# Kernel optimization log

Measured on AMD Instinct MI355X. Metric: run time of the kernel, lower is better.

The kernel has to match this reference:

```python
import jax, jax.numpy as jnp
import numpy as np

D_MODEL = 1024
HEAD = 16
D_K = D_MODEL // HEAD


def setup_inputs() -> dict:
    key = jax.random.key(0)
    ks = jax.random.split(key, 6)
    B, S = 2, 2048
    scale = 1.0 / np.sqrt(D_MODEL)
    return {
        "q": jax.random.normal(ks[0], (B, S, D_MODEL), dtype=jnp.float32),
        "k": jax.random.normal(ks[1], (B, S, D_MODEL), dtype=jnp.float32),
        "v": jax.random.normal(ks[2], (B, S, D_MODEL), dtype=jnp.float32),
        "W_q": jax.random.normal(ks[3], (D_MODEL, D_MODEL), dtype=jnp.float32) * scale,
        "W_k": jax.random.normal(ks[4], (D_MODEL, D_MODEL), dtype=jnp.float32) * scale,
        "W_v": jax.random.normal(ks[5], (D_MODEL, D_MODEL), dtype=jnp.float32) * scale,
    }


def reference(q, k, v, W_q, W_k, W_v):
    B, S, _ = q.shape
    # nn.Linear: y = x @ W.T ; then split heads (B,S,H,dk) -> (B,H,S,dk) -> (B*H,S,dk)
    def proj(x, W):
        y = jnp.einsum('bsd,ed->bse', x, W)
        return y.reshape(B, S, HEAD, D_K).transpose(0, 2, 1, 3).reshape(B * HEAD, S, D_K)

    qh = proj(q, W_q)
    kh = proj(k, W_k)
    vh = proj(v, W_v)

    scores = jnp.einsum('nsd,ntd->nst', qh, kh) / np.sqrt(D_K).astype(np.float32)
    attn = jax.nn.softmax(scores, axis=2)
    out = jnp.einsum('nst,ntd->nsd', attn, vh)  # (B*H, S, dk), flat index = b*H + h

    # Faithful torch.chunk(dim=0, head) + torch.cat(dim=2):
    # chunk c = rows [c*B:(c+1)*B]; concatenated along feature dim.
    out = out.reshape(HEAD, B, S, D_K).transpose(1, 2, 0, 3).reshape(B, S, D_MODEL)
    return out
```

## Files before the change

### kernel.cpp

```cpp
#include <hip/hip_runtime.h>
#include <hip/hip_bf16.h>
#include <stdint.h>

typedef unsigned short u16;
typedef __attribute__((ext_vector_type(8))) short bf16x8;
typedef __attribute__((ext_vector_type(8))) _Float16 f16x8;
typedef __attribute__((ext_vector_type(4))) float f32x4;
typedef __attribute__((ext_vector_type(4))) u16 u16x4;
typedef __attribute__((ext_vector_type(4))) float f4v;

#define DEV __device__ __forceinline__

DEV u16 f2bf(float x) {
    union { float f; uint32_t u; } v; v.f = x;
    uint32_t r = v.u + 0x7FFF + ((v.u >> 16) & 1);
    return (u16)(r >> 16);
}

DEV float fexp2(float x) {
    float r;
    asm("v_exp_f32 %0, %1" : "=v"(r) : "v"(x));
    return r;
}

DEV f32x4 mfma16(bf16x8 a, bf16x8 b, f32x4 c) {
    return __builtin_amdgcn_mfma_f32_16x16x32_bf16(a, b, c, 0, 0, 0);
}
DEV f32x4 mfma16h(f16x8 a, f16x8 b, f32x4 c) {
    return __builtin_amdgcn_mfma_f32_16x16x32_f16(a, b, c, 0, 0, 0);
}

DEV void gld_lds16(const u16* g, u16* lds) {
    __builtin_amdgcn_global_load_lds(
        (const __attribute__((address_space(1))) void*)g,
        (__attribute__((address_space(3))) void*)lds, 16, 0, 0);
}

#define VMCNT2 asm volatile("s_waitcnt vmcnt(2)" ::: "memory")
#define VMCNT0 asm volatile("s_waitcnt vmcnt(0)" ::: "memory")
#define BAR() __builtin_amdgcn_s_barrier()

DEV u16 h2u(_Float16 h) { union { _Float16 h; u16 u; } v; v.h = h; return v.u; }

struct PrepArgs {
    const float* src[6];
    u16* dst[6];
    int n4[6];
};

__global__ __launch_bounds__(256) void prep_kernel(PrepArgs a) {
    const int z = blockIdx.y;
    const f4v* __restrict__ src = (const f4v*)a.src[z];
    u16x4* __restrict__ dst = (u16x4*)a.dst[z];
    const int n4 = a.n4[z];
    int i = blockIdx.x * blockDim.x + threadIdx.x;
    const int stride = gridDim.x * blockDim.x;
    for (; i < n4; i += stride) {
        f4v x = src[i];
        u16x4 d;
#pragma unroll
        for (int c = 0; c < 4; ++c) d[c] = h2u((_Float16)x[c]);
        dst[i] = d;
    }
}

struct ProjArgs {
    const u16* xf[3];
    const u16* wf[3];
    u16* outq;
    u16* outk;
    u16* outvt;
};

__global__ __launch_bounds__(512, 2) void proj_kernel(ProjArgs args) {
    __shared__ u16 lds[2][32768];

    const int tid = threadIdx.x;
    const int w = tid >> 6, l = tid & 63;
    const int fr = l & 15, fg = l >> 4;
    const int wa = w >> 2, wb = w & 3;

    const int b0 = blockIdx.x;
    const int swz = (b0 & 7) * 24 + (b0 >> 3);
    const int z = swz >> 6;
    const int r = swz & 63;

    int ta, tb;
    const u16 *A0, *B0;
    if (z < 2) {
        ta = r & 3; tb = r >> 2;
        A0 = args.wf[z];
        B0 = args.xf[z];
    } else {
        ta = r >> 2; tb = r & 3;
        A0 = args.xf[2];
        B0 = args.wf[2];
    }

    const int s_r = tid >> 3;
    const int s_c = (((tid & 7) ^ (s_r & 7)) << 3);
    const size_t aoff = (size_t)(ta * 256 + s_r) * 1024 + s_c;
    const size_t boff = (size_t)(tb * 256 + s_r) * 1024 + s_c;

    const int abase = (wa * 128 + fr) * 64;
    const int bbase = 16384 + (wb * 64 + fr) * 64;
    const int sl0 = ((fg) ^ (fr & 7)) << 3;
    const int sl1 = ((4 + fg) ^ (fr & 7)) << 3;

    f32x4 acc[8][4];
#pragma unroll
    for (int mi = 0; mi < 8; ++mi)
#pragma unroll
        for (int ni = 0; ni < 4; ++ni)
            acc[mi][ni] = (f32x4){0.f, 0.f, 0.f, 0.f};

#define STAGE2(SRC, OFFBASE, REGION, HALF, BUFN, KTN)                               \
    do {                                                                            \
        _Pragma("unroll")                                                           \
        for (int j = 0; j < 2; ++j) {                                               \
            gld_lds16((SRC) + (OFFBASE) + (size_t)((HALF) * 128 + j * 64) * 1024    \
                           + (size_t)(KTN) * 64,                                    \
                      &lds[BUFN][(REGION) + (HALF) * 8192 + j * 4096 + w * 512]);   \
        }                                                                           \
    } while (0)

#pragma unroll
    for (int h = 0; h < 2; ++h) {
#pragma unroll
        for (int j = 0; j < 2; ++j) {
            gld_lds16(A0 + aoff + (size_t)(h * 128 + j * 64) * 1024,
                      &lds[0][h * 8192 + j * 4096 + w * 512]);
            gld_lds16(B0 + boff + (size_t)(h * 128 + j * 64) * 1024,
                      &lds[0][16384 + h * 8192 + j * 4096 + w * 512]);
        }
    }

#define PHASE(MQ0, STAGECALL)                                                       \
    do {                                                                            \
        if (more) STAGECALL;                                                        \
        f16x8 p00 = *(const f16x8*)&Lb[abase + (MQ0) * 1024 + sl0];                 \
        f16x8 p01 = *(const f16x8*)&Lb[abase + (MQ0) * 1024 + sl1];                 \
        f16x8 p10 = *(const f16x8*)&Lb[abase + (MQ0 + 1) * 1024 + sl0];             \
        f16x8 p11 = *(const f16x8*)&Lb[abase + (MQ0 + 1) * 1024 + sl1];             \
        BAR();                                                                      \
        __builtin_amdgcn_s_setprio(1);                                              \
        _Pragma("unroll")                                                           \
        for (int ni = 0; ni < 4; ++ni) {                                            \
            acc[MQ0][ni] = mfma16h(p00, Bf0[ni], acc[MQ0][ni]);                     \
            acc[MQ0][ni] = mfma16h(p01, Bf1[ni], acc[MQ0][ni]);                     \
            acc[MQ0 + 1][ni] = mfma16h(p10, Bf0[ni], acc[MQ0 + 1][ni]);             \
            acc[MQ0 + 1][ni] = mfma16h(p11, Bf1[ni], acc[MQ0 + 1][ni]);             \
        }                                                                           \
        __builtin_amdgcn_s_setprio(0);                                              \
        BAR();                                                                      \
    } while (0)

#pragma unroll 1
    for (int t = 0; t < 16; ++t) {
        const int buf = t & 1;
        const int nbuf = buf ^ 1;
        const int tn = t + 1;
        const bool more = (tn < 16);
        const int ktn = tn;
        const u16* An = A0;
        const u16* Bn = B0;
        const u16* Lb = &lds[buf][0];

        f16x8 Bf0[4], Bf1[4];

        if (more) STAGE2(An, aoff, 0, 0, nbuf, ktn);
        if (more) { VMCNT2; } else { VMCNT0; }
        BAR();
        {
            f16x8 a00 = *(const f16x8*)&Lb[abase + sl0];
            f16x8 a01 = *(const f16x8*)&Lb[abase + sl1];
            f16x8 a10 = *(const f16x8*)&Lb[abase + 1024 + sl0];
            f16x8 a11 = *(const f16x8*)&Lb[abase + 1024 + sl1];
#pragma unroll
            for (int ni = 0; ni < 4; ++ni) {
                Bf0[ni] = *(const f16x8*)&Lb[bbase + ni * 1024 + sl0];
                Bf1[ni] = *(const f16x8*)&Lb[bbase + ni * 1024 + sl1];
            }
            BAR();
            __builtin_amdgcn_s_setprio(1);
#pragma unroll
            for (int ni = 0; ni < 4; ++ni) {
                acc[0][ni] = mfma16h(a00, Bf0[ni], acc[0][ni]);
                acc[0][ni] = mfma16h(a01, Bf1[ni], acc[0][ni]);
                acc[1][ni] = mfma16h(a10, Bf0[ni], acc[1][ni]);
                acc[1][ni] = mfma16h(a11, Bf1[ni], acc[1][ni]);
            }
            __builtin_amdgcn_s_setprio(0);
            BAR();
        }
        PHASE(2, STAGE2(An, aoff, 0, 1, nbuf, ktn));
        PHASE(4, STAGE2(Bn, boff, 16384, 0, nbuf, ktn));
        PHASE(6, STAGE2(Bn, boff, 16384, 1, nbuf, ktn));
    }
#undef PHASE
#undef STAGE2

    if (z < 2) {
        u16* outp = (z == 0) ? args.outq : args.outk;
        const float osc = (z == 0) ? 0.18033688011112f : 1.0f;
#pragma unroll
        for (int mq = 0; mq < 8; ++mq) {
#pragma unroll
            for (int ni = 0; ni < 4; ++ni) {
                const int e0 = ta * 256 + wa * 128 + mq * 16 + fg * 4;
                const int m = tb * 256 + wb * 64 + ni * 16 + fr;
                const int n = (m >> 11) * 16 + (e0 >> 6);
                const int s = m & 2047;
                u16x4 pk;
#pragma unroll
                for (int rr = 0; rr < 4; ++rr) pk[rr] = f2bf(acc[mq][ni][rr] * osc);
                *(u16x4*)&outp[((size_t)(n * 2048 + s)) * 64 + (e0 & 63)] = pk;
            }
        }
    } else {
        u16* outp = args.outvt;
#pragma unroll
        for (int mq = 0; mq < 8; ++mq) {
#pragma unroll
            for (int ni = 0; ni < 4; ++ni) {
                const int m0 = ta * 256 + wa * 128 + mq * 16 + fg * 4;
                const int e = tb * 256 + wb * 64 + ni * 16 + fr;
                const int n = (m0 >> 11) * 16 + (e >> 6);
                u16x4 pk;
#pragma unroll
                for (int rr = 0; rr < 4; ++rr) pk[rr] = f2bf(acc[mq][ni][rr]);
                *(u16x4*)&outp[((size_t)(n * 64 + (e & 63))) * 2048 + (m0 & 2047)] = pk;
            }
        }
    }
}

__global__ __launch_bounds__(512, 8) void attn_kernel(const u16* __restrict__ qh,
                                                      const u16* __restrict__ kh,
                                                      const u16* __restrict__ vt,
                                                      float* __restrict__ out) {
    __shared__ u16 lds[2][8192];

    const int tid = threadIdx.x;
    const int w = tid >> 6, l = tid & 63;
    const int fr = l & 15, fg = l >> 4;

    const int b = blockIdx.x;
    const int n = (b & 7) * 4 + ((b >> 3) >> 4);
    const int qt = (b >> 3) & 15;
    const int qbase = qt * 128 + w * 16;

    const u16* khn = kh + (size_t)n * 2048 * 64;
    const u16* vtn = vt + (size_t)n * 64 * 2048;

    const u16* qrow = qh + ((size_t)n * 2048 + qbase + fr) * 64;
    bf16x8 aq0 = *(const bf16x8*)(qrow + fg * 8);
    bf16x8 aq1 = *(const bf16x8*)(qrow + 32 + fg * 8);

    const int srow = tid >> 3;
    const int sch = tid & 7;
    const int kg_s = (srow & 3) + 4 * ((srow >> 3) & 1);
    const int kws = ((sch + kg_s) & 7) * 8;
    const int vg_s = srow & 7;
    const int vws = ((sch + vg_s) & 7) * 8;

    const int rbase = ((fr >> 2) << 3) + (fr & 3);
    const int kg_r = (fr & 3) + 4 * ((fr >> 2) & 1);
    const int ksl0 = ((fg + kg_r) & 7) * 8;
    const int ksl1 = ((fg + 4 + kg_r) & 7) * 8;
    const int vg_r = fr & 7;
    const int vsl0 = ((fg + vg_r) & 7) * 8;
    const int vsl1 = ((4 + fg + vg_r) & 7) * 8;

    f32x4 acc[4];
#pragma unroll
    for (int dc = 0; dc < 4; ++dc) acc[dc] = (f32x4){0.f, 0.f, 0.f, 0.f};
    float lsum = 0.f;

    bf16x8 kr0, vr0;

#define STAGE_LOAD(c_) do {                                                        \
        kr0 = *(const bf16x8*)(khn + (size_t)((c_) * 64 + srow) * 64 + sch * 8);   \
        vr0 = *(const bf16x8*)(vtn + (size_t)srow * 2048 + (c_) * 64 + sch * 8);   \
    } while (0)

#define STAGE_WRITE(buf_) do {                                                     \
        *(bf16x8*)&lds[buf_][srow * 64 + kws] = kr0;                               \
        *(bf16x8*)&lds[buf_][4096 + srow * 64 + vws] = vr0;                        \
    } while (0)

    STAGE_LOAD(0);
    STAGE_WRITE(0);
    STAGE_LOAD(1);
    __syncthreads();

    for (int c = 0; c < 32; ++c) {
        const int cur = c & 1;
        const u16* Kb = &lds[cur][0];
        const u16* Vb = &lds[cur][4096];

        f32x4 sf[4];
        __builtin_amdgcn_s_setprio(1);
#pragma unroll
        for (int cc = 0; cc < 4; ++cc) {
            const int rr = ((cc >> 1) << 5) + ((cc & 1) << 2) + rbase;
            f32x4 s = (f32x4){0.f, 0.f, 0.f, 0.f};
            s = mfma16(*(const bf16x8*)&Kb[rr * 64 + ksl0], aq0, s);
            s = mfma16(*(const bf16x8*)&Kb[rr * 64 + ksl1], aq1, s);
            sf[cc] = s;
        }
        __builtin_amdgcn_s_setprio(0);

        f32x4 ps = (f32x4){0.f, 0.f, 0.f, 0.f};
#pragma unroll
        for (int cc = 0; cc < 4; ++cc) {
#pragma unroll
            for (int rr = 0; rr < 4; ++rr)
                sf[cc][rr] = fexp2(sf[cc][rr]);
            ps += sf[cc];
        }
        lsum += (ps[0] + ps[1]) + (ps[2] + ps[3]);

        if (c < 31) {
            STAGE_WRITE(cur ^ 1);
            if (c < 30) STAGE_LOAD(c + 2);
        }

        __builtin_amdgcn_s_setprio(1);
#pragma unroll
        for (int pw = 0; pw < 2; ++pw) {
            union { bf16x8 v; uint32_t u[4]; } ap;
#pragma unroll
            for (int q2 = 0; q2 < 4; ++q2) {
                float lo = sf[2 * pw + (q2 >> 1)][(q2 & 1) * 2 + 0];
                float hi = sf[2 * pw + (q2 >> 1)][(q2 & 1) * 2 + 1];
                asm("v_cvt_pk_bf16_f32 %0, %1, %2" : "=v"(ap.u[q2]) : "v"(lo), "v"(hi));
            }
            const int vsl = pw ? vsl1 : vsl0;
#pragma unroll
            for (int dc = 0; dc < 4; ++dc)
                acc[dc] = mfma16(*(const bf16x8*)&Vb[(dc * 16 + fr) * 64 + vsl],
                                 ap.v, acc[dc]);
        }
        __builtin_amdgcn_s_setprio(0);

        if (c < 31) __syncthreads();
    }

    lsum += __shfl_xor(lsum, 16, 64);
    lsum += __shfl_xor(lsum, 32, 64);

    const float inv = 1.f / lsum;
    const int bq = n & 1;
    const int col0 = (n >> 1) * 64;
    float* orow = out + ((size_t)bq * 2048 + qbase + fr) * 1024 + col0 + fg * 4;
#pragma unroll
    for (int dblk = 0; dblk < 4; ++dblk) {
        f4v o;
#pragma unroll
        for (int rr = 0; rr < 4; ++rr) o[rr] = acc[dblk][rr] * inv;
        *(f4v*)&orow[dblk * 16] = o;
    }
#undef STAGE_LOAD
#undef STAGE_WRITE
}

extern "C" void kernel_launch(void* const* d_in, const int* in_sizes, int n_in,
                              void* d_out, int out_size, void* d_ws, size_t ws_size,
                              hipStream_t stream) {
    (void)n_in; (void)out_size; (void)ws_size;
    const float* q  = (const float*)d_in[0];
    const float* k  = (const float*)d_in[1];
    const float* v  = (const float*)d_in[2];
    const float* Wq = (const float*)d_in[3];
    const float* Wk = (const float*)d_in[4];
    const float* Wv = (const float*)d_in[5];

    uint8_t* ws = (uint8_t*)d_ws;
    const size_t MB = 1024ull * 1024ull;
    u16* xq_f = (u16*)(ws + 0 * MB);
    u16* xk_f = (u16*)(ws + 8 * MB);
    u16* xv_f = (u16*)(ws + 16 * MB);
    u16* wq_f = (u16*)(ws + 24 * MB);
    u16* wk_f = (u16*)(ws + 26 * MB);
    u16* wv_f = (u16*)(ws + 28 * MB);
    u16* qh   = (u16*)(ws + 30 * MB);
    u16* kh   = (u16*)(ws + 38 * MB);
    u16* vt   = (u16*)(ws + 46 * MB);

    PrepArgs pp;
    pp.src[0] = q;  pp.src[1] = k;  pp.src[2] = v;
    pp.src[3] = Wq; pp.src[4] = Wk; pp.src[5] = Wv;
    pp.dst[0] = xq_f; pp.dst[1] = xk_f; pp.dst[2] = xv_f;
    pp.dst[3] = wq_f; pp.dst[4] = wk_f; pp.dst[5] = wv_f;
    pp.n4[0] = pp.n4[1] = pp.n4[2] = in_sizes[0] / 4;
    pp.n4[3] = pp.n4[4] = pp.n4[5] = in_sizes[3] / 4;
    prep_kernel<<<dim3(1024, 6), 256, 0, stream>>>(pp);

    ProjArgs pa;
    pa.xf[0] = xq_f; pa.xf[1] = xk_f; pa.xf[2] = xv_f;
    pa.wf[0] = wq_f; pa.wf[1] = wk_f; pa.wf[2] = wv_f;
    pa.outq = qh; pa.outk = kh; pa.outvt = vt;
    proj_kernel<<<dim3(192), 512, 0, stream>>>(pa);

    attn_kernel<<<dim3(512), 512, 0, stream>>>(qh, kh, vt, (float*)d_out);
}
```

Before: 99.86 us.

## Split attention key range across two blocks and merge partial results

```diff
diff --git a/kernel.cpp b/kernel.cpp
--- a/kernel.cpp
+++ b/kernel.cpp
@@ -238,7 +238,8 @@
 __global__ __launch_bounds__(512, 8) void attn_kernel(const u16* __restrict__ qh,
                                                       const u16* __restrict__ kh,
                                                       const u16* __restrict__ vt,
-                                                      float* __restrict__ out) {
+                                                      float* __restrict__ num,
+                                                      float* __restrict__ lbuf) {
     __shared__ u16 lds[2][8192];
 
     const int tid = threadIdx.x;
@@ -246,12 +247,16 @@
     const int fr = l & 15, fg = l >> 4;
 
     const int b = blockIdx.x;
-    const int n = (b & 7) * 4 + ((b >> 3) >> 4);
-    const int qt = (b >> 3) & 15;
+    const int xcd = b & 7;
+    const int j = b >> 3;
+    const int n = xcd * 4 + (j >> 5);
+    const int rem = j & 31;
+    const int qt = rem >> 1;
+    const int g = rem & 1;
     const int qbase = qt * 128 + w * 16;
 
-    const u16* khn = kh + (size_t)n * 2048 * 64;
-    const u16* vtn = vt + (size_t)n * 64 * 2048;
+    const u16* khn = kh + ((size_t)n * 2048 + g * 1024) * 64;
+    const u16* vtn = vt + (size_t)n * 64 * 2048 + g * 1024;
 
     const u16* qrow = qh + ((size_t)n * 2048 + qbase + fr) * 64;
     bf16x8 aq0 = *(const bf16x8*)(qrow + fg * 8);
@@ -294,7 +299,7 @@
     STAGE_LOAD(1);
     __syncthreads();
 
-    for (int c = 0; c < 32; ++c) {
+    for (int c = 0; c < 16; ++c) {
         const int cur = c & 1;
         const u16* Kb = &lds[cur][0];
         const u16* Vb = &lds[cur][4096];
@@ -321,9 +326,9 @@
         }
         lsum += (ps[0] + ps[1]) + (ps[2] + ps[3]);
 
-        if (c < 31) {
+        if (c < 15) {
             STAGE_WRITE(cur ^ 1);
-            if (c < 30) STAGE_LOAD(c + 2);
+            if (c < 14) STAGE_LOAD(c + 2);
         }
 
         __builtin_amdgcn_s_setprio(1);
@@ -344,25 +349,41 @@
         }
         __builtin_amdgcn_s_setprio(0);
 
-        if (c < 31) __syncthreads();
+        if (c < 15) __syncthreads();
     }
 
     lsum += __shfl_xor(lsum, 16, 64);
     lsum += __shfl_xor(lsum, 32, 64);
 
-    const float inv = 1.f / lsum;
-    const int bq = n & 1;
-    const int col0 = (n >> 1) * 64;
-    float* orow = out + ((size_t)bq * 2048 + qbase + fr) * 1024 + col0 + fg * 4;
-#pragma unroll
-    for (int dblk = 0; dblk < 4; ++dblk) {
-        f4v o;
-#pragma unroll
-        for (int rr = 0; rr < 4; ++rr) o[rr] = acc[dblk][rr] * inv;
-        *(f4v*)&orow[dblk * 16] = o;
-    }
+    float* nump = num + ((((size_t)g * 32 + n) * 2048 + qbase + fr)) * 64 + fg * 4;
+#pragma unroll
+    for (int dblk = 0; dblk < 4; ++dblk)
+        *(f4v*)&nump[dblk * 16] = acc[dblk];
+    if (fg == 0)
+        lbuf[((size_t)g * 32 + n) * 2048 + qbase + fr] = lsum;
 #undef STAGE_LOAD
 #undef STAGE_WRITE
+}
+
+__global__ __launch_bounds__(256) void merge_kernel(const float* __restrict__ num,
+                                                    const float* __restrict__ lbuf,
+                                                    float* __restrict__ out) {
+    const int i = blockIdx.x * 256 + threadIdx.x;
+    const int n = i >> 15;
+    const int rem = i & 32767;
+    const int row = rem >> 4;
+    const int dq4 = rem & 15;
+
+    const size_t o0 = ((size_t)(n * 2048 + row)) * 16 + dq4;
+    const size_t o1 = o0 + (size_t)32 * 2048 * 16;
+    f4v a = ((const f4v*)num)[o0];
+    f4v b = ((const f4v*)num)[o1];
+    const float lt = lbuf[n * 2048 + row] + lbuf[32 * 2048 + n * 2048 + row];
+    const float inv = 1.f / lt;
+    f4v o;
+#pragma unroll
+    for (int rr = 0; rr < 4; ++rr) o[rr] = (a[rr] + b[rr]) * inv;
+    *(f4v*)&out[((size_t)((n & 1) * 2048 + row)) * 1024 + (n >> 1) * 64 + dq4 * 4] = o;
 }
 
 extern "C" void kernel_launch(void* const* d_in, const int* in_sizes, int n_in,
@@ -384,9 +405,11 @@
     u16* wq_f = (u16*)(ws + 24 * MB);
     u16* wk_f = (u16*)(ws + 26 * MB);
     u16* wv_f = (u16*)(ws + 28 * MB);
-    u16* qh   = (u16*)(ws + 30 * MB);
-    u16* kh   = (u16*)(ws + 38 * MB);
-    u16* vt   = (u16*)(ws + 46 * MB);
+    float* num  = (float*)(ws + 0 * MB);
+    u16* qh   = (u16*)(ws + 32 * MB);
+    u16* kh   = (u16*)(ws + 40 * MB);
+    u16* vt   = (u16*)(ws + 48 * MB);
+    float* lbuf = (float*)(ws + 56 * MB);
 
     PrepArgs pp;
     pp.src[0] = q;  pp.src[1] = k;  pp.src[2] = v;
@@ -403,5 +426,7 @@
     pa.outq = qh; pa.outk = kh; pa.outvt = vt;
     proj_kernel<<<dim3(192), 512, 0, stream>>>(pa);
 
-    attn_kernel<<<dim3(512), 512, 0, stream>>>(qh, kh, vt, (float*)d_out);
-}
+    attn_kernel<<<dim3(1024), 512, 0, stream>>>(qh, kh, vt, num, lbuf);
+
+    merge_kernel<<<dim3(4096), 256, 0, stream>>>(num, lbuf, (float*)d_out);
+}
```

Result: slower. 113.8 us (+13.9%).
